# Kernel tuning notes

Measured on AMD Instinct MI355X. Metric: run time of the kernel, lower is better.

## Reference

```python
import jax, jax.numpy as jnp
import numpy as np

B, D, S, K = 4096, 256, 32, 32
TEMP = 1.0

def _unit(x):
    return x / jnp.linalg.norm(x, axis=-1, keepdims=True)

def setup_inputs() -> dict:
    key = jax.random.key(0)
    k1, k2, k3, k4 = jax.random.split(key, 4)
    return {
        "embeddings": _unit(jax.random.normal(k1, (B, D), dtype=jnp.float32)),
        "similar_malicious_embeddings": _unit(jax.random.normal(k2, (B, S, D), dtype=jnp.float32)),
        "diverse_malicious_embeddings": _unit(jax.random.normal(k3, (B, K, D), dtype=jnp.float32)),
        "labels": jax.random.randint(k4, (B,), 0, 2, dtype=jnp.int64),
    }

def reference(embeddings, similar_malicious_embeddings, diverse_malicious_embeddings, labels):
    b = embeddings.shape[0]
    # all pairwise sims zi . zj / T  -> [B, B]
    sims = jnp.matmul(embeddings, embeddings.T) / TEMP
    # sims of zi vs its own similar/diverse sets -> [B, S], [B, K]
    sim_s = jnp.einsum('bd,bsd->bs', embeddings, similar_malicious_embeddings) / TEMP
    sim_d = jnp.einsum('bd,bkd->bk', embeddings, diverse_malicious_embeddings) / TEMP
    not_self = ~jnp.eye(b, dtype=bool)
    # denominator over c_xi = (all embeddings except i) + similar_i + diverse_i
    denom = (jnp.exp(sims) * not_self).sum(-1) + jnp.exp(sim_s).sum(-1) + jnp.exp(sim_d).sum(-1)
    mal = labels == 1
    # d_xi = malicious others (b1_xi) + similar_i + diverse_i
    b1_mask = mal[None, :] & not_self  # [B, B]
    sum_num = (sims * b1_mask).sum(-1) + sim_s.sum(-1) + sim_d.sum(-1)
    cnt = b1_mask.sum(-1) + sim_s.shape[1] + sim_d.shape[1]  # |d_xi| per i (>0 since S,K>0)
    # per zp: -log(exp(s_zp)/denom); averaged over d_xi
    per_i = -sum_num / cnt.astype(sims.dtype) + jnp.log(denom)
    loss = jnp.where(mal, per_i, 0.0).sum() / b
    return loss
```

## Files before the change

### kernel.cpp

```cpp
#include <hip/hip_runtime.h>
#include <stdint.h>

#define BTOT 4096
#define DD   256
#define SS   32
#define KKN  32
#define NGEMM 528

typedef unsigned short u16;
using f32x4  = __attribute__((ext_vector_type(4))) float;
using bf16x8 = __attribute__((ext_vector_type(8))) short;

__device__ __forceinline__ u16 f2bf(float f) {
    uint32_t u = __builtin_bit_cast(uint32_t, f);
    u = (u + 0x7FFFu + ((u >> 16) & 1u)) >> 16;
    return (u16)u;
}
__device__ __forceinline__ float bf2f(u16 h) {
    uint32_t u = ((uint32_t)h) << 16;
    return __builtin_bit_cast(float, u);
}

__global__ __launch_bounds__(256) void cast_kernel(const float* __restrict__ E,
                                                   u16* __restrict__ ebf) {
    int idx = blockIdx.x * 256 + threadIdx.x;
    const float4* p = reinterpret_cast<const float4*>(E) + (size_t)idx * 2;
    float4 a = p[0], b = p[1];
    uint4 o;
    o.x = (uint32_t)f2bf(a.x) | ((uint32_t)f2bf(a.y) << 16);
    o.y = (uint32_t)f2bf(a.z) | ((uint32_t)f2bf(a.w) << 16);
    o.z = (uint32_t)f2bf(b.x) | ((uint32_t)f2bf(b.y) << 16);
    o.w = (uint32_t)f2bf(b.z) | ((uint32_t)f2bf(b.w) << 16);
    reinterpret_cast<uint4*>(ebf)[idx] = o;
}

__global__ __launch_bounds__(256) void gemm_kernel(
    const u16* __restrict__ ebf, const int* __restrict__ labels,
    float* __restrict__ gden, float* __restrict__ gnum)
{
    __shared__ u16 As[128 * 32];
    __shared__ u16 Bs[128 * 32];
    __shared__ float rbuf[2][2][128];
    __shared__ float cbuf[2][2][128];

    int bid = blockIdx.x;
    int R = (int)((65.0f - sqrtf(4225.0f - 8.0f * (float)bid)) * 0.5f);
    while (R > 0 && R * (65 - R) / 2 > bid) --R;
    while ((R + 1) * (64 - R) / 2 <= bid) ++R;
    int C = R + (bid - R * (65 - R) / 2);

    int brow = R * 128, bcol = C * 128;
    int t = threadIdx.x, w = t >> 6, lane = t & 63;
    int wr = w >> 1, wc = w & 1;
    int r16 = lane & 15, hi = lane >> 4;
    int kq = hi * 8;

    f32x4 acc[4][4] = {};

    for (int kt = 0; kt < DD / 32; ++kt) {
        int k0 = kt * 32;
        #pragma unroll
        for (int it = 0; it < 2; ++it) {
            int c   = t + 256 * it;
            int row = c >> 2;
            int col = (c & 3) * 8;
            const u16* ga = &ebf[(size_t)(brow + row) * DD + k0 + col];
            const u16* gb = &ebf[(size_t)(bcol + row) * DD + k0 + col];
            __builtin_amdgcn_global_load_lds(
                (const __attribute__((address_space(1))) unsigned int*)ga,
                (__attribute__((address_space(3))) unsigned int*)&As[c * 8], 16, 0, 0);
            __builtin_amdgcn_global_load_lds(
                (const __attribute__((address_space(1))) unsigned int*)gb,
                (__attribute__((address_space(3))) unsigned int*)&Bs[c * 8], 16, 0, 0);
        }
        __syncthreads();

        bf16x8 af[4], bfr[4];
        #pragma unroll
        for (int m = 0; m < 4; ++m)
            af[m] = *(const bf16x8*)&As[(wr * 64 + m * 16 + r16) * 32 + kq];
        #pragma unroll
        for (int n = 0; n < 4; ++n)
            bfr[n] = *(const bf16x8*)&Bs[(wc * 64 + n * 16 + r16) * 32 + kq];
        #pragma unroll
        for (int m = 0; m < 4; ++m)
            #pragma unroll
            for (int n = 0; n < 4; ++n)
                acc[m][n] = __builtin_amdgcn_mfma_f32_16x16x32_bf16(af[m], bfr[n], acc[m][n], 0, 0, 0);
        __syncthreads();
    }

    bool offdiag = (C != R);

    float malf[4];
    #pragma unroll
    for (int n = 0; n < 4; ++n)
        malf[n] = (float)labels[bcol + wc * 64 + n * 16 + r16];
    float malr[16];
    #pragma unroll
    for (int m = 0; m < 4; ++m)
        #pragma unroll
        for (int r = 0; r < 4; ++r)
            malr[m * 4 + r] = (float)labels[brow + wr * 64 + m * 16 + hi * 4 + r];

    float cd[4] = {0.f, 0.f, 0.f, 0.f}, cn[4] = {0.f, 0.f, 0.f, 0.f};

    #pragma unroll
    for (int m = 0; m < 4; ++m) {
        #pragma unroll
        for (int r = 0; r < 4; ++r) {
            float pe = 0.f, pn = 0.f;
            #pragma unroll
            for (int n = 0; n < 4; ++n) {
                float v  = acc[m][n][r];
                float ex = __expf(v);
                pe += ex;
                pn += malf[n] * v;
                cd[n] += ex;
                cn[n] += malr[m * 4 + r] * v;
            }
            #pragma unroll
            for (int s = 1; s < 16; s <<= 1) {
                pe += __shfl_xor(pe, s, 64);
                pn += __shfl_xor(pn, s, 64);
            }
            if (r16 == 0) {
                int rl = wr * 64 + m * 16 + hi * 4 + r;
                rbuf[0][wc][rl] = pe;
                rbuf[1][wc][rl] = pn;
            }
        }
    }

    if (offdiag) {
        #pragma unroll
        for (int n = 0; n < 4; ++n) {
            cd[n] += __shfl_xor(cd[n], 16, 64);
            cd[n] += __shfl_xor(cd[n], 32, 64);
            cn[n] += __shfl_xor(cn[n], 16, 64);
            cn[n] += __shfl_xor(cn[n], 32, 64);
            if (lane < 16) {
                int cl = wc * 64 + n * 16 + lane;
                cbuf[0][wr][cl] = cd[n];
                cbuf[1][wr][cl] = cn[n];
            }
        }
    }
    __syncthreads();

    if (t < 128) {
        int i = brow + t;
        gden[(size_t)i * 32 + C] = rbuf[0][0][t] + rbuf[0][1][t];
        gnum[(size_t)i * 32 + C] = rbuf[1][0][t] + rbuf[1][1][t];
    } else if (offdiag) {
        int tt = t - 128;
        int j = bcol + tt;
        gden[(size_t)j * 32 + R] = cbuf[0][0][tt] + cbuf[0][1][tt];
        gnum[(size_t)j * 32 + R] = cbuf[1][0][tt] + cbuf[1][1][tt];
    }
}

__global__ __launch_bounds__(256, 4) void simdiv_kernel(
    const float* __restrict__ E, const float* __restrict__ Sim, const float* __restrict__ Div,
    float* __restrict__ sdpart)
{
    int i    = blockIdx.x * 4 + (threadIdx.x >> 6);
    int lane = threadIdx.x & 63;
    int g = lane >> 4, sub = lane & 15;

    const char* Eb = (const char*)(E + (size_t)i * DD);
    float4 e0 = *(const float4*)(Eb + 0 * 256 + sub * 16);
    float4 e1 = *(const float4*)(Eb + 1 * 256 + sub * 16);
    float4 e2 = *(const float4*)(Eb + 2 * 256 + sub * 16);
    float4 e3 = *(const float4*)(Eb + 3 * 256 + sub * 16);

    const char* Sb = (const char*)(Sim + (size_t)i * SS * DD) + g * 1024 + sub * 16;
    const char* Db = (const char*)(Div + (size_t)i * KKN * DD) + g * 1024 + sub * 16;

    float4 buf[4][4];
    float accs = 0.f, acce = 0.f;

#define ISSUE(SET)                                                                  \
    {                                                                               \
        const char* b_ = ((SET) < 8) ? (Sb + (SET) * 4096) : (Db + ((SET) - 8) * 4096); \
        buf[(SET) & 3][0] = *(const float4*)(b_ + 0);                               \
        buf[(SET) & 3][1] = *(const float4*)(b_ + 256);                             \
        buf[(SET) & 3][2] = *(const float4*)(b_ + 512);                             \
        buf[(SET) & 3][3] = *(const float4*)(b_ + 768);                             \
    }

#define COMPUTE(SET)                                                                \
    {                                                                               \
        float4 s0 = buf[(SET) & 3][0], s1 = buf[(SET) & 3][1];                      \
        float4 s2 = buf[(SET) & 3][2], s3 = buf[(SET) & 3][3];                      \
        float d = e0.x * s0.x + e0.y * s0.y + e0.z * s0.z + e0.w * s0.w             \
                + e1.x * s1.x + e1.y * s1.y + e1.z * s1.z + e1.w * s1.w             \
                + e2.x * s2.x + e2.y * s2.y + e2.z * s2.z + e2.w * s2.w             \
                + e3.x * s3.x + e3.y * s3.y + e3.z * s3.z + e3.w * s3.w;            \
        d += __shfl_xor(d, 1, 64);                                                  \
        d += __shfl_xor(d, 2, 64);                                                  \
        d += __shfl_xor(d, 4, 64);                                                  \
        d += __shfl_xor(d, 8, 64);                                                  \
        accs += d;                                                                  \
        acce += __expf(d);                                                          \
    }

    ISSUE(0) ISSUE(1) ISSUE(2) ISSUE(3)
    COMPUTE(0)  ISSUE(4)
    COMPUTE(1)  ISSUE(5)
    COMPUTE(2)  ISSUE(6)
    COMPUTE(3)  ISSUE(7)
    COMPUTE(4)  ISSUE(8)
    COMPUTE(5)  ISSUE(9)
    COMPUTE(6)  ISSUE(10)
    COMPUTE(7)  ISSUE(11)
    COMPUTE(8)  ISSUE(12)
    COMPUTE(9)  ISSUE(13)
    COMPUTE(10) ISSUE(14)
    COMPUTE(11) ISSUE(15)
    COMPUTE(12)
    COMPUTE(13)
    COMPUTE(14)
    COMPUTE(15)
#undef ISSUE
#undef COMPUTE

    accs += __shfl_xor(accs, 16, 64);
    accs += __shfl_xor(accs, 32, 64);
    acce += __shfl_xor(acce, 16, 64);
    acce += __shfl_xor(acce, 32, 64);

    float sd = 0.f;
    {
        float c;
        c = bf2f(f2bf(e0.x)); sd += c * c;  c = bf2f(f2bf(e0.y)); sd += c * c;
        c = bf2f(f2bf(e0.z)); sd += c * c;  c = bf2f(f2bf(e0.w)); sd += c * c;
        c = bf2f(f2bf(e1.x)); sd += c * c;  c = bf2f(f2bf(e1.y)); sd += c * c;
        c = bf2f(f2bf(e1.z)); sd += c * c;  c = bf2f(f2bf(e1.w)); sd += c * c;
        c = bf2f(f2bf(e2.x)); sd += c * c;  c = bf2f(f2bf(e2.y)); sd += c * c;
        c = bf2f(f2bf(e2.z)); sd += c * c;  c = bf2f(f2bf(e2.w)); sd += c * c;
        c = bf2f(f2bf(e3.x)); sd += c * c;  c = bf2f(f2bf(e3.y)); sd += c * c;
        c = bf2f(f2bf(e3.z)); sd += c * c;  c = bf2f(f2bf(e3.w)); sd += c * c;
    }
    sd += __shfl_xor(sd, 1, 64);
    sd += __shfl_xor(sd, 2, 64);
    sd += __shfl_xor(sd, 4, 64);
    sd += __shfl_xor(sd, 8, 64);

    if (lane == 0) {
        float4 o; o.x = accs; o.y = acce; o.z = sd; o.w = 0.f;
        *(float4*)(sdpart + (size_t)i * 4) = o;
    }
}

__global__ __launch_bounds__(128) void reduce1_kernel(
    const int* __restrict__ labels, const float* __restrict__ gden,
    const float* __restrict__ gnum, const float* __restrict__ sdpart,
    float* __restrict__ part)
{
    __shared__ float sA[128], sB[128];
    __shared__ int   sC[128];
    int p = blockIdx.x, t = threadIdx.x;
    int i = p * 128 + t;

    const float4* dr = reinterpret_cast<const float4*>(gden + (size_t)i * 32);
    const float4* nr = reinterpret_cast<const float4*>(gnum + (size_t)i * 32);
    float4 sp = *(const float4*)(sdpart + (size_t)i * 4);

    float num = sp.x;
    float den = sp.y;
    float sdv = sp.z;
    int lab = labels[i];
    den -= __expf(sdv);
    num -= lab ? sdv : 0.f;

    #pragma unroll
    for (int c = 0; c < 8; ++c) {
        float4 a = dr[c]; den += a.x + a.y + a.z + a.w;
        float4 b = nr[c]; num += b.x + b.y + b.z + b.w;
    }
    sA[t] = lab ? __logf(den) : 0.f;
    sB[t] = lab ? num : 0.f;
    sC[t] = lab;
    __syncthreads();
    for (int s = 64; s > 0; s >>= 1) {
        if (t < s) { sA[t] += sA[t + s]; sB[t] += sB[t + s]; sC[t] += sC[t + s]; }
        __syncthreads();
    }
    if (t == 0) {
        part[p]      = sA[0];
        part[32 + p] = sB[0];
        part[64 + p] = (float)sC[0];
    }
}

__global__ __launch_bounds__(64) void final_kernel(const float* __restrict__ part,
                                                   float* __restrict__ out)
{
    int lane = threadIdx.x;
    float lg = (lane < 32) ? part[lane]      : 0.f;
    float nm = (lane < 32) ? part[32 + lane] : 0.f;
    float ml = (lane < 32) ? part[64 + lane] : 0.f;
    #pragma unroll
    for (int s = 1; s < 64; s <<= 1) {
        lg += __shfl_xor(lg, s, 64);
        nm += __shfl_xor(nm, s, 64);
        ml += __shfl_xor(ml, s, 64);
    }
    if (lane == 0) {
        float cnt = ml - 1.f + (float)(SS + KKN);
        out[0] = (lg - nm / cnt) / (float)BTOT;
    }
}

extern "C" void kernel_launch(void* const* d_in, const int* in_sizes, int n_in,
                              void* d_out, int out_size, void* d_ws, size_t ws_size,
                              hipStream_t stream) {
    const float* E   = (const float*)d_in[0];
    const float* Sim = (const float*)d_in[1];
    const float* Div = (const float*)d_in[2];
    const int* labels = (const int*)d_in[3];
    float* out = (float*)d_out;

    char* ws = (char*)d_ws;
    u16*   ebf    = (u16*)ws;   ws += (size_t)BTOT * DD * sizeof(u16);
    float* gden   = (float*)ws; ws += (size_t)BTOT * 32 * sizeof(float);
    float* gnum   = (float*)ws; ws += (size_t)BTOT * 32 * sizeof(float);
    float* sdpart = (float*)ws; ws += (size_t)BTOT * 4 * sizeof(float);
    float* part   = (float*)ws;

    cast_kernel<<<BTOT * DD / 8 / 256, 256, 0, stream>>>(E, ebf);
    gemm_kernel<<<NGEMM, 256, 0, stream>>>(ebf, labels, gden, gnum);
    simdiv_kernel<<<BTOT / 4, 256, 0, stream>>>(E, Sim, Div, sdpart);
    reduce1_kernel<<<32, 128, 0, stream>>>(labels, gden, gnum, sdpart, part);
    final_kernel<<<1, 64, 0, stream>>>(part, out);
}
```

Baseline: 76.10 us.

## Merge GEMM and sim/div kernels into one interleaved launch

Folds the compute-bound MFMA Gram-matrix kernel and the bandwidth-bound similar/diverse dot-product kernel into a single launch. Every third block runs a GEMM tile and the other two handle four rows of sim/div. The goal is to overlap tensor-core work with streaming HBM reads on the same CUs and save one launch. The merged kernel loses the (256,4) launch bound the sim/div path had, and its register and LDS footprint is set by the GEMM branch, which may reduce occupancy for the memory-bound blocks.

```diff
diff --git a/kernel.cpp b/kernel.cpp
--- a/kernel.cpp
+++ b/kernel.cpp
@@ -6,6 +6,7 @@
 #define SS   32
 #define KKN  32
 #define NGEMM 528
+#define NBLK  (NGEMM * 3)
 
 typedef unsigned short u16;
 using f32x4  = __attribute__((ext_vector_type(4))) float;
@@ -34,151 +35,153 @@
     reinterpret_cast<uint4*>(ebf)[idx] = o;
 }
 
-__global__ __launch_bounds__(256) void gemm_kernel(
+__global__ __launch_bounds__(256) void fat_kernel(
+    const float* __restrict__ E, const float* __restrict__ Sim, const float* __restrict__ Div,
     const u16* __restrict__ ebf, const int* __restrict__ labels,
-    float* __restrict__ gden, float* __restrict__ gnum)
+    float* __restrict__ gden, float* __restrict__ gnum, float* __restrict__ sdpart)
 {
     __shared__ u16 As[128 * 32];
     __shared__ u16 Bs[128 * 32];
     __shared__ float rbuf[2][2][128];
     __shared__ float cbuf[2][2][128];
 
-    int bid = blockIdx.x;
-    int R = (int)((65.0f - sqrtf(4225.0f - 8.0f * (float)bid)) * 0.5f);
-    while (R > 0 && R * (65 - R) / 2 > bid) --R;
-    while ((R + 1) * (64 - R) / 2 <= bid) ++R;
-    int C = R + (bid - R * (65 - R) / 2);
-
-    int brow = R * 128, bcol = C * 128;
-    int t = threadIdx.x, w = t >> 6, lane = t & 63;
-    int wr = w >> 1, wc = w & 1;
-    int r16 = lane & 15, hi = lane >> 4;
-    int kq = hi * 8;
-
-    f32x4 acc[4][4] = {};
-
-    for (int kt = 0; kt < DD / 32; ++kt) {
-        int k0 = kt * 32;
+    int bid  = blockIdx.x;
+    int t    = threadIdx.x;
+    int w    = t >> 6;
+    int lane = t & 63;
+
+    if (bid % 3 == 2) {
+        int g = bid / 3;
+        int R = (int)((65.0f - sqrtf(4225.0f - 8.0f * (float)g)) * 0.5f);
+        while (R > 0 && R * (65 - R) / 2 > g) --R;
+        while ((R + 1) * (64 - R) / 2 <= g) ++R;
+        int C = R + (g - R * (65 - R) / 2);
+
+        int brow = R * 128, bcol = C * 128;
+        int wr = w >> 1, wc = w & 1;
+        int r16 = lane & 15, hi = lane >> 4;
+        int kq = hi * 8;
+
+        f32x4 acc[4][4] = {};
+
+        for (int kt = 0; kt < DD / 32; ++kt) {
+            int k0 = kt * 32;
+            #pragma unroll
+            for (int it = 0; it < 2; ++it) {
+                int c   = t + 256 * it;
+                int row = c >> 2;
+                int col = (c & 3) * 8;
+                const u16* ga = &ebf[(size_t)(brow + row) * DD + k0 + col];
+                const u16* gb = &ebf[(size_t)(bcol + row) * DD + k0 + col];
+                __builtin_amdgcn_global_load_lds(
+                    (const __attribute__((address_space(1))) unsigned int*)ga,
+                    (__attribute__((address_space(3))) unsigned int*)&As[c * 8], 16, 0, 0);
+                __builtin_amdgcn_global_load_lds(
+                    (const __attribute__((address_space(1))) unsigned int*)gb,
+                    (__attribute__((address_space(3))) unsigned int*)&Bs[c * 8], 16, 0, 0);
+            }
+            __syncthreads();
+
+            bf16x8 af[4], bfr[4];
+            #pragma unroll
+            for (int m = 0; m < 4; ++m)
+                af[m] = *(const bf16x8*)&As[(wr * 64 + m * 16 + r16) * 32 + kq];
+            #pragma unroll
+            for (int n = 0; n < 4; ++n)
+                bfr[n] = *(const bf16x8*)&Bs[(wc * 64 + n * 16 + r16) * 32 + kq];
+            #pragma unroll
+            for (int m = 0; m < 4; ++m)
+                #pragma unroll
+                for (int n = 0; n < 4; ++n)
+                    acc[m][n] = __builtin_amdgcn_mfma_f32_16x16x32_bf16(af[m], bfr[n], acc[m][n], 0, 0, 0);
+            __syncthreads();
+        }
+
+        bool offdiag = (C != R);
+
+        float malf[4];
         #pragma unroll
-        for (int it = 0; it < 2; ++it) {
-            int c   = t + 256 * it;
-            int row = c >> 2;
-            int col = (c & 3) * 8;
-            const u16* ga = &ebf[(size_t)(brow + row) * DD + k0 + col];
-            const u16* gb = &ebf[(size_t)(bcol + row) * DD + k0 + col];
-            __builtin_amdgcn_global_load_lds(
-                (const __attribute__((address_space(1))) unsigned int*)ga,
-                (__attribute__((address_space(3))) unsigned int*)&As[c * 8], 16, 0, 0);
-            __builtin_amdgcn_global_load_lds(
-                (const __attribute__((address_space(1))) unsigned int*)gb,
-                (__attribute__((address_space(3))) unsigned int*)&Bs[c * 8], 16, 0, 0);
-        }
-        __syncthreads();
-
-        bf16x8 af[4], bfr[4];
+        for (int n = 0; n < 4; ++n)
+            malf[n] = (float)labels[bcol + wc * 64 + n * 16 + r16];
+        float malr[16];
         #pragma unroll
         for (int m = 0; m < 4; ++m)
-            af[m] = *(const bf16x8*)&As[(wr * 64 + m * 16 + r16) * 32 + kq];
+            #pragma unroll
+            for (int r = 0; r < 4; ++r)
+                malr[m * 4 + r] = (float)labels[brow + wr * 64 + m * 16 + hi * 4 + r];
+
+        float cd[4] = {0.f, 0.f, 0.f, 0.f}, cn[4] = {0.f, 0.f, 0.f, 0.f};
+
         #pragma unroll
-        for (int n = 0; n < 4; ++n)
-            bfr[n] = *(const bf16x8*)&Bs[(wc * 64 + n * 16 + r16) * 32 + kq];
-        #pragma unroll
-        for (int m = 0; m < 4; ++m)
-            #pragma unroll
-            for (int n = 0; n < 4; ++n)
-                acc[m][n] = __builtin_amdgcn_mfma_f32_16x16x32_bf16(af[m], bfr[n], acc[m][n], 0, 0, 0);
+        for (int m = 0; m < 4; ++m) {
+            #pragma unroll
+            for (int r = 0; r < 4; ++r) {
+                float pe = 0.f, pn = 0.f;
+                #pragma unroll
+                for (int n = 0; n < 4; ++n) {
+                    float v  = acc[m][n][r];
+                    float ex = __expf(v);
+                    pe += ex;
+                    pn += malf[n] * v;
+                    cd[n] += ex;
+                    cn[n] += malr[m * 4 + r] * v;
+                }
+                #pragma unroll
+                for (int s = 1; s < 16; s <<= 1) {
+                    pe += __shfl_xor(pe, s, 64);
+                    pn += __shfl_xor(pn, s, 64);
+                }
+                if (r16 == 0) {
+                    int rl = wr * 64 + m * 16 + hi * 4 + r;
+                    rbuf[0][wc][rl] = pe;
+                    rbuf[1][wc][rl] = pn;
+                }
+            }
+        }
+
+        if (offdiag) {
+            #pragma unroll
+            for (int n = 0; n < 4; ++n) {
+                cd[n] += __shfl_xor(cd[n], 16, 64);
+                cd[n] += __shfl_xor(cd[n], 32, 64);
+                cn[n] += __shfl_xor(cn[n], 16, 64);
+                cn[n] += __shfl_xor(cn[n], 32, 64);
+                if (lane < 16) {
+                    int cl = wc * 64 + n * 16 + lane;
+                    cbuf[0][wr][cl] = cd[n];
+                    cbuf[1][wr][cl] = cn[n];
+                }
+            }
+        }
         __syncthreads();
-    }
-
-    bool offdiag = (C != R);
-
-    float malf[4];
-    #pragma unroll
-    for (int n = 0; n < 4; ++n)
-        malf[n] = (float)labels[bcol + wc * 64 + n * 16 + r16];
-    float malr[16];
-    #pragma unroll
-    for (int m = 0; m < 4; ++m)
-        #pragma unroll
-        for (int r = 0; r < 4; ++r)
-            malr[m * 4 + r] = (float)labels[brow + wr * 64 + m * 16 + hi * 4 + r];
-
-    float cd[4] = {0.f, 0.f, 0.f, 0.f}, cn[4] = {0.f, 0.f, 0.f, 0.f};
-
-    #pragma unroll
-    for (int m = 0; m < 4; ++m) {
-        #pragma unroll
-        for (int r = 0; r < 4; ++r) {
-            float pe = 0.f, pn = 0.f;
-            #pragma unroll
-            for (int n = 0; n < 4; ++n) {
-                float v  = acc[m][n][r];
-                float ex = __expf(v);
-                pe += ex;
-                pn += malf[n] * v;
-                cd[n] += ex;
-                cn[n] += malr[m * 4 + r] * v;
-            }
-            #pragma unroll
-            for (int s = 1; s < 16; s <<= 1) {
-                pe += __shfl_xor(pe, s, 64);
-                pn += __shfl_xor(pn, s, 64);
-            }
-            if (r16 == 0) {
-                int rl = wr * 64 + m * 16 + hi * 4 + r;
-                rbuf[0][wc][rl] = pe;
-                rbuf[1][wc][rl] = pn;
-            }
-        }
-    }
-
-    if (offdiag) {
-        #pragma unroll
-        for (int n = 0; n < 4; ++n) {
-            cd[n] += __shfl_xor(cd[n], 16, 64);
-            cd[n] += __shfl_xor(cd[n], 32, 64);
-            cn[n] += __shfl_xor(cn[n], 16, 64);
-            cn[n] += __shfl_xor(cn[n], 32, 64);
-            if (lane < 16) {
-                int cl = wc * 64 + n * 16 + lane;
-                cbuf[0][wr][cl] = cd[n];
-                cbuf[1][wr][cl] = cn[n];
-            }
-        }
-    }
-    __syncthreads();
-
-    if (t < 128) {
-        int i = brow + t;
-        gden[(size_t)i * 32 + C] = rbuf[0][0][t] + rbuf[0][1][t];
-        gnum[(size_t)i * 32 + C] = rbuf[1][0][t] + rbuf[1][1][t];
-    } else if (offdiag) {
-        int tt = t - 128;
-        int j = bcol + tt;
-        gden[(size_t)j * 32 + R] = cbuf[0][0][tt] + cbuf[0][1][tt];
-        gnum[(size_t)j * 32 + R] = cbuf[1][0][tt] + cbuf[1][1][tt];
-    }
-}
-
-__global__ __launch_bounds__(256, 4) void simdiv_kernel(
-    const float* __restrict__ E, const float* __restrict__ Sim, const float* __restrict__ Div,
-    float* __restrict__ sdpart)
-{
-    int i    = blockIdx.x * 4 + (threadIdx.x >> 6);
-    int lane = threadIdx.x & 63;
-    int g = lane >> 4, sub = lane & 15;
-
-    const char* Eb = (const char*)(E + (size_t)i * DD);
-    float4 e0 = *(const float4*)(Eb + 0 * 256 + sub * 16);
-    float4 e1 = *(const float4*)(Eb + 1 * 256 + sub * 16);
-    float4 e2 = *(const float4*)(Eb + 2 * 256 + sub * 16);
-    float4 e3 = *(const float4*)(Eb + 3 * 256 + sub * 16);
-
-    const char* Sb = (const char*)(Sim + (size_t)i * SS * DD) + g * 1024 + sub * 16;
-    const char* Db = (const char*)(Div + (size_t)i * KKN * DD) + g * 1024 + sub * 16;
-
-    float4 buf[4][4];
-    float accs = 0.f, acce = 0.f;
+
+        if (t < 128) {
+            int i = brow + t;
+            gden[(size_t)i * 32 + C] = rbuf[0][0][t] + rbuf[0][1][t];
+            gnum[(size_t)i * 32 + C] = rbuf[1][0][t] + rbuf[1][1][t];
+        } else if (offdiag) {
+            int tt = t - 128;
+            int j = bcol + tt;
+            gden[(size_t)j * 32 + R] = cbuf[0][0][tt] + cbuf[0][1][tt];
+            gnum[(size_t)j * 32 + R] = cbuf[1][0][tt] + cbuf[1][1][tt];
+        }
+    } else {
+        int sid = bid - bid / 3;
+        if (sid >= BTOT / 4) return;
+        int i = sid * 4 + w;
+        int g = lane >> 4, sub = lane & 15;
+
+        const char* Eb = (const char*)(E + (size_t)i * DD);
+        float4 e0 = *(const float4*)(Eb + 0 * 256 + sub * 16);
+        float4 e1 = *(const float4*)(Eb + 1 * 256 + sub * 16);
+        float4 e2 = *(const float4*)(Eb + 2 * 256 + sub * 16);
+        float4 e3 = *(const float4*)(Eb + 3 * 256 + sub * 16);
+
+        const char* Sb = (const char*)(Sim + (size_t)i * SS * DD) + g * 1024 + sub * 16;
+        const char* Db = (const char*)(Div + (size_t)i * KKN * DD) + g * 1024 + sub * 16;
+
+        float4 buf[4][4];
+        float accs = 0.f, acce = 0.f;
 
 #define ISSUE(SET)                                                                  \
     {                                                                               \
@@ -205,51 +208,52 @@
         acce += __expf(d);                                                          \
     }
 
-    ISSUE(0) ISSUE(1) ISSUE(2) ISSUE(3)
-    COMPUTE(0)  ISSUE(4)
-    COMPUTE(1)  ISSUE(5)
-    COMPUTE(2)  ISSUE(6)
-    COMPUTE(3)  ISSUE(7)
-    COMPUTE(4)  ISSUE(8)
-    COMPUTE(5)  ISSUE(9)
-    COMPUTE(6)  ISSUE(10)
-    COMPUTE(7)  ISSUE(11)
-    COMPUTE(8)  ISSUE(12)
-    COMPUTE(9)  ISSUE(13)
-    COMPUTE(10) ISSUE(14)
-    COMPUTE(11) ISSUE(15)
-    COMPUTE(12)
-    COMPUTE(13)
-    COMPUTE(14)
-    COMPUTE(15)
+        ISSUE(0) ISSUE(1) ISSUE(2) ISSUE(3)
+        COMPUTE(0)  ISSUE(4)
+        COMPUTE(1)  ISSUE(5)
+        COMPUTE(2)  ISSUE(6)
+        COMPUTE(3)  ISSUE(7)
+        COMPUTE(4)  ISSUE(8)
+        COMPUTE(5)  ISSUE(9)
+        COMPUTE(6)  ISSUE(10)
+        COMPUTE(7)  ISSUE(11)
+        COMPUTE(8)  ISSUE(12)
+        COMPUTE(9)  ISSUE(13)
+        COMPUTE(10) ISSUE(14)
+        COMPUTE(11) ISSUE(15)
+        COMPUTE(12)
+        COMPUTE(13)
+        COMPUTE(14)
+        COMPUTE(15)
 #undef ISSUE
 #undef COMPUTE
 
-    accs += __shfl_xor(accs, 16, 64);
-    accs += __shfl_xor(accs, 32, 64);
-    acce += __shfl_xor(acce, 16, 64);
-    acce += __shfl_xor(acce, 32, 64);
-
-    float sd = 0.f;
-    {
-        float c;
-        c = bf2f(f2bf(e0.x)); sd += c * c;  c = bf2f(f2bf(e0.y)); sd += c * c;
-        c = bf2f(f2bf(e0.z)); sd += c * c;  c = bf2f(f2bf(e0.w)); sd += c * c;
-        c = bf2f(f2bf(e1.x)); sd += c * c;  c = bf2f(f2bf(e1.y)); sd += c * c;
-        c = bf2f(f2bf(e1.z)); sd += c * c;  c = bf2f(f2bf(e1.w)); sd += c * c;
-        c = bf2f(f2bf(e2.x)); sd += c * c;  c = bf2f(f2bf(e2.y)); sd += c * c;
-        c = bf2f(f2bf(e2.z)); sd += c * c;  c = bf2f(f2bf(e2.w)); sd += c * c;
-        c = bf2f(f2bf(e3.x)); sd += c * c;  c = bf2f(f2bf(e3.y)); sd += c * c;
-        c = bf2f(f2bf(e3.z)); sd += c * c;  c = bf2f(f2bf(e3.w)); sd += c * c;
-    }
-    sd += __shfl_xor(sd, 1, 64);
-    sd += __shfl_xor(sd, 2, 64);
-    sd += __shfl_xor(sd, 4, 64);
-    sd += __shfl_xor(sd, 8, 64);
-
-    if (lane == 0) {
-        float4 o; o.x = accs; o.y = acce; o.z = sd; o.w = 0.f;
-        *(float4*)(sdpart + (size_t)i * 4) = o;
+        accs += __shfl_xor(accs, 16, 64);
+        accs += __shfl_xor(accs, 32, 64);
+        acce += __shfl_xor(acce, 16, 64);
+        acce += __shfl_xor(acce, 32, 64);
+
+        float sd = 0.f;
+        {
+            float c;
+            c = bf2f(f2bf(e0.x)); sd += c * c;  c = bf2f(f2bf(e0.y)); sd += c * c;
+            c = bf2f(f2bf(e0.z)); sd += c * c;  c = bf2f(f2bf(e0.w)); sd += c * c;
+            c = bf2f(f2bf(e1.x)); sd += c * c;  c = bf2f(f2bf(e1.y)); sd += c * c;
+            c = bf2f(f2bf(e1.z)); sd += c * c;  c = bf2f(f2bf(e1.w)); sd += c * c;
+            c = bf2f(f2bf(e2.x)); sd += c * c;  c = bf2f(f2bf(e2.y)); sd += c * c;
+            c = bf2f(f2bf(e2.z)); sd += c * c;  c = bf2f(f2bf(e2.w)); sd += c * c;
+            c = bf2f(f2bf(e3.x)); sd += c * c;  c = bf2f(f2bf(e3.y)); sd += c * c;
+            c = bf2f(f2bf(e3.z)); sd += c * c;  c = bf2f(f2bf(e3.w)); sd += c * c;
+        }
+        sd += __shfl_xor(sd, 1, 64);
+        sd += __shfl_xor(sd, 2, 64);
+        sd += __shfl_xor(sd, 4, 64);
+        sd += __shfl_xor(sd, 8, 64);
+
+        if (lane == 0) {
+            float4 o; o.x = accs; o.y = acce; o.z = sd; o.w = 0.f;
+            *(float4*)(sdpart + (size_t)i * 4) = o;
+        }
     }
 }
 
@@ -330,8 +334,7 @@
     float* part   = (float*)ws;
 
     cast_kernel<<<BTOT * DD / 8 / 256, 256, 0, stream>>>(E, ebf);
-    gemm_kernel<<<NGEMM, 256, 0, stream>>>(ebf, labels, gden, gnum);
-    simdiv_kernel<<<BTOT / 4, 256, 0, stream>>>(E, Sim, Div, sdpart);
+    fat_kernel<<<NBLK, 256, 0, stream>>>(E, Sim, Div, ebf, labels, gden, gnum, sdpart);
     reduce1_kernel<<<32, 128, 0, stream>>>(labels, gden, gnum, sdpart, part);
     final_kernel<<<1, 64, 0, stream>>>(part, out);
 }
```

Measured after the change: 65.63 us (median of 2 runs). 13.7% less time.
